# Optimization experiments

Hardware: AMD Instinct MI355X
Metric: run time of the kernel (lower is better)

Reference implementation:

```python
import jax, jax.numpy as jnp
import numpy as np

EPS = 1e-12  # torch f.normalize eps


def _rms_norm(x, g):
    # f.normalize(x, dim=1) * g * sqrt(C): L2-normalize over channel dim
    c = x.shape[1]
    n = jnp.maximum(jnp.linalg.norm(x, axis=1, keepdims=True), EPS)
    return x / n * g * (c ** 0.5)


def setup_inputs() -> dict:
    key = jax.random.key(0)
    ks = jax.random.split(key, 5)
    b, dim, H, W = 32, 256, 64, 64
    heads, dim_head, num_mem = 4, 32, 4
    hidden = heads * dim_head
    return {
        "x": jax.random.normal(ks[0], (b, dim, H, W), dtype=jnp.float32),
        "g1": jnp.ones((1, dim, 1, 1), dtype=jnp.float32),
        "mem_kv": jax.random.normal(ks[1], (2, heads, dim_head, num_mem), dtype=jnp.float32),
        "w_qkv": jax.random.normal(ks[2], (3 * hidden, dim), dtype=jnp.float32) * (1.0 / np.sqrt(dim)),
        "w_out": jax.random.normal(ks[3], (dim, hidden), dtype=jnp.float32) * (1.0 / np.sqrt(hidden)),
        "b_out": jnp.zeros((dim,), dtype=jnp.float32),
        "g2": jnp.ones((1, dim, 1, 1), dtype=jnp.float32),
    }


def reference(x, g1, mem_kv, w_qkv, w_out, b_out, g2):
    b, c, H, W = x.shape
    _, heads, dim_head, num_mem = mem_kv.shape
    n = H * W
    scale = dim_head ** -0.5

    xn = _rms_norm(x, g1)
    # 1x1 conv qkv projection: [b, 3*hidden, H, W]
    qkv = jnp.einsum('oc,bchw->bohw', w_qkv, xn)
    hidden = heads * dim_head
    q, k, v = jnp.split(qkv, 3, axis=1)
    # b (h d) x y -> b h d (x y)
    q = q.reshape(b, heads, dim_head, n)
    k = k.reshape(b, heads, dim_head, n)
    v = v.reshape(b, heads, dim_head, n)

    mk = jnp.broadcast_to(mem_kv[0], (b, heads, dim_head, num_mem))
    mv = jnp.broadcast_to(mem_kv[1], (b, heads, dim_head, num_mem))
    k = jnp.concatenate([mk, k], axis=-1)
    v = jnp.concatenate([mv, v], axis=-1)

    q = jax.nn.softmax(q, axis=-2) * scale  # softmax over head dim d
    k = jax.nn.softmax(k, axis=-1)          # softmax over sequence n

    context = jnp.einsum('bhdn,bhen->bhde', k, v)   # [b,h,d,e]
    out = jnp.einsum('bhde,bhdn->bhen', context, q)  # [b,h,e,n]
    out = out.reshape(b, hidden, H, W)

    o = jnp.einsum('oc,bchw->bohw', w_out, out) + b_out[None, :, None, None]
    return _rms_norm(o, g2)
```

## Files before the change

### kernel.cpp

```cpp
#include <hip/hip_runtime.h>
#include <math.h>

#define CC   256
#define HW   4096
#define OC3  384
#define HID  128
#define DH   32
#define NM   4
#define NPART 8
#define SCALE 0.17677669529663688f

typedef __bf16 bf16x8 __attribute__((ext_vector_type(8)));
typedef float  f32x4  __attribute__((ext_vector_type(4)));

__device__ __forceinline__ ushort f2bf(float x) {
    union { float f; unsigned u; } v; v.f = x;
    unsigned r = v.u + 0x7fffu + ((v.u >> 16) & 1u);
    return (ushort)(r >> 16);
}
__device__ __forceinline__ float bf2f(ushort b) {
    union { unsigned u; float f; } v; v.u = ((unsigned)b) << 16; return v.f;
}
__device__ __forceinline__ void g2l16(const void* g, void* l) {
    __builtin_amdgcn_global_load_lds(
        (const __attribute__((address_space(1))) void*)g,
        (__attribute__((address_space(3))) void*)l, 16, 0, 0);
}

__global__ __launch_bounds__(256) void k_xn(const float* __restrict__ x,
        const float* __restrict__ wqkv, const float* __restrict__ g1,
        const float* __restrict__ wout,
        ushort* __restrict__ wq2t, ushort* __restrict__ woutt,
        ushort* __restrict__ xnT) {
    __shared__ float xt[256 * 36];
    __shared__ float ps[8 * 33];
    __shared__ float invn[32];
    int tid = threadIdx.x;
    if (blockIdx.x < 384) {
        int o = blockIdx.x;
        wq2t[(size_t)o * CC + tid] = f2bf(wqkv[(size_t)o * CC + tid] * g1[tid] * 16.0f);
        if (o < CC && tid < HID) woutt[(size_t)o * HID + tid] = f2bf(wout[(size_t)o * HID + tid]);
    }
    int pix0 = blockIdx.x * 32;
    int b = pix0 >> 12, hw0 = pix0 & 4095;
    int p = tid & 31, cg = tid >> 5;
    const float* xb = x + (size_t)b * CC * HW + hw0;
    {
        int cr = tid >> 3;
        int chunk = tid & 7;
        #pragma unroll
        for (int pass = 0; pass < 8; ++pass) {
            int c = pass * 32 + cr;
            float4 v = *(const float4*)&xb[(size_t)c * HW + chunk * 4];
            *(float4*)&xt[c * 36 + chunk * 4] = v;
        }
    }
    __syncthreads();
    float s = 0.f;
    #pragma unroll 8
    for (int i = 0; i < 32; ++i) { float v = xt[(cg * 32 + i) * 36 + p]; s += v * v; }
    ps[cg * 33 + p] = s;
    __syncthreads();
    if (tid < 32) {
        float t = 0.f;
        #pragma unroll
        for (int g = 0; g < 8; ++g) t += ps[g * 33 + tid];
        invn[tid] = 1.0f / fmaxf(sqrtf(t), 1e-12f);
    }
    __syncthreads();
    float inv = invn[p];
    ushort* dst = xnT + ((size_t)(pix0 + p)) * CC + cg * 32;
    #pragma unroll
    for (int q = 0; q < 4; ++q) {
        uint4 pk; ushort* o8 = (ushort*)&pk;
        #pragma unroll
        for (int i = 0; i < 8; ++i) o8[i] = f2bf(xt[(cg * 32 + q * 8 + i) * 36 + p] * inv);
        *(uint4*)&dst[q * 8] = pk;
    }
}

__global__ __launch_bounds__(256) void k_qkv(const ushort* __restrict__ wq2t,
        const ushort* __restrict__ xnT, ushort* __restrict__ qkv) {
    __shared__ __align__(16) ushort As[2][128 * 32];
    __shared__ __align__(16) ushort Bs[2][128 * 32];
    int tid = threadIdx.x;
    int lin = blockIdx.x + 2 * (blockIdx.y + 32 * blockIdx.z);
    int swz = (lin & 7) * 256 + (lin >> 3);
    int m0 = 128 + (swz % 2) * 128;
    int t_ = swz / 2;
    int p0 = (t_ & 31) * 128;
    int b  = t_ >> 5;
    int lane = tid & 63, wid = tid >> 6;
    int l15 = tid & 15, quad = (tid >> 4) & 3;
    int wm = wid >> 1, wn = wid & 1;
    int rsub = lane >> 2;
    const ushort* Ab = wq2t + (size_t)m0 * CC;
    const ushort* Bb = xnT + ((size_t)(b * HW + p0)) * CC;
    f32x4 acc[4][4];
    #pragma unroll
    for (int i = 0; i < 4; ++i)
        #pragma unroll
        for (int j = 0; j < 4; ++j) acc[i][j] = (f32x4){0.f, 0.f, 0.f, 0.f};

    auto stage = [&](int buf, int k0) {
        #pragma unroll
        for (int q = 0; q < 2; ++q) {
            int rw = wid * 32 + q * 16;
            int r  = rw + rsub;
            int sc = (lane & 3) ^ ((r >> 1) & 3);
            g2l16(Ab + (size_t)r * CC + k0 + sc * 8, &As[buf][rw * 32]);
            g2l16(Bb + (size_t)r * CC + k0 + sc * 8, &Bs[buf][rw * 32]);
        }
    };

    stage(0, 0);
    __syncthreads();
    #pragma unroll
    for (int s = 0; s < 8; ++s) {
        int cur = s & 1;
        if (s < 7) stage(cur ^ 1, (s + 1) * 32);
        bf16x8 af[4], bfr[4];
        #pragma unroll
        for (int mt = 0; mt < 4; ++mt) {
            int ra = wm * 64 + mt * 16 + l15;
            af[mt] = *(const bf16x8*)&As[cur][ra * 32 + ((quad ^ ((ra >> 1) & 3)) << 3)];
        }
        #pragma unroll
        for (int nt = 0; nt < 4; ++nt) {
            int rb = wn * 64 + nt * 16 + l15;
            bfr[nt] = *(const bf16x8*)&Bs[cur][rb * 32 + ((quad ^ ((rb >> 1) & 3)) << 3)];
        }
        #pragma unroll
        for (int mt = 0; mt < 4; ++mt)
            #pragma unroll
            for (int nt = 0; nt < 4; ++nt)
                acc[mt][nt] = __builtin_amdgcn_mfma_f32_16x16x32_bf16(
                                  af[mt], bfr[nt], acc[mt][nt], 0, 0, 0);
        __syncthreads();
    }
    #pragma unroll
    for (int mt = 0; mt < 4; ++mt) {
        int o = m0 + wm * 64 + mt * 16 + quad * 4;
        #pragma unroll
        for (int nt = 0; nt < 4; ++nt) {
            int pix = p0 + wn * 64 + nt * 16 + l15;
            ushort* dst = qkv + ((size_t)(b * OC3 + o)) * HW + pix;
            #pragma unroll
            for (int r = 0; r < 4; ++r) dst[(size_t)r * HW] = f2bf(acc[mt][nt][r]);
        }
    }
}

__global__ void k_ksoft(const ushort* __restrict__ qkv, const float* __restrict__ memkv,
                        float* __restrict__ kmaxb, float* __restrict__ rsumb) {
    int row = blockIdx.x * 4 + (threadIdx.x >> 6);
    int lane = threadIdx.x & 63;
    int b = row >> 7, hd = row & 127;
    const ushort* kp = qkv + ((size_t)(b * OC3 + HID + hd)) * HW;
    uint4 kreg[8];
    #pragma unroll
    for (int i = 0; i < 8; ++i) kreg[i] = *(const uint4*)&kp[i * 512 + lane * 8];
    float m = -1e30f;
    #pragma unroll
    for (int i = 0; i < 8; ++i) {
        const ushort* e = (const ushort*)&kreg[i];
        #pragma unroll
        for (int j = 0; j < 8; ++j) m = fmaxf(m, bf2f(e[j]));
    }
    #pragma unroll
    for (int s = 1; s < 64; s <<= 1) m = fmaxf(m, __shfl_xor(m, s));
    const float* mk = memkv + hd * NM;
    #pragma unroll
    for (int j = 0; j < NM; ++j) m = fmaxf(m, mk[j]);
    float s = 0.f;
    #pragma unroll
    for (int i = 0; i < 8; ++i) {
        const ushort* e = (const ushort*)&kreg[i];
        #pragma unroll
        for (int j = 0; j < 8; ++j) s += __expf(bf2f(e[j]) - m);
    }
    #pragma unroll
    for (int t = 1; t < 64; t <<= 1) s += __shfl_xor(s, t);
    #pragma unroll
    for (int j = 0; j < NM; ++j) s += __expf(mk[j] - m);
    if (lane == 0) { kmaxb[row] = m; rsumb[row] = 1.0f / s; }
}

__global__ __launch_bounds__(256) void k_ctx(const ushort* __restrict__ qkv,
        const float* __restrict__ memkv, const float* __restrict__ kmaxb,
        const float* __restrict__ rsumb, float* __restrict__ ctxp) {
    __shared__ __align__(16) char smem[32768];
    ushort* klw = (ushort*)smem;
    ushort* vlw = (ushort*)(smem + 16384);
    float*  red = (float*)smem;
    int tid = threadIdx.x;
    int lane = tid & 63, wid = tid >> 6;
    int l15 = lane & 15, quad = lane >> 4;
    int bh = blockIdx.x, part = blockIdx.y;
    int b = bh >> 2, h = bh & 3;
    int rowbase = bh * DH;
    int r  = lane >> 1;
    int ch = (lane & 1) * 32;
    const ushort* kp = qkv + ((size_t)(b * OC3 + HID + h * DH) + r) * HW + part * 512;
    const ushort* vp = qkv + ((size_t)(b * OC3 + 2 * HID + h * DH) + r) * HW + part * 512;
    float kmr = kmaxb[rowbase + r], rsr = rsumb[rowbase + r];
    ushort* myk = klw + wid * 2048;
    ushort* myv = vlw + wid * 2048;
    f32x4 acc[2][2];
    #pragma unroll
    for (int i = 0; i < 2; ++i)
        #pragma unroll
        for (int j = 0; j < 2; ++j) acc[i][j] = (f32x4){0.f, 0.f, 0.f, 0.f};

    #pragma unroll
    for (int t = 0; t < 2; ++t) {
        int n0 = wid * 64 + t * 256;
        #pragma unroll
        for (int i = 0; i < 4; ++i) {
            uint4 kv4 = *(const uint4*)&kp[n0 + ch + i * 8];
            uint4 vv4 = *(const uint4*)&vp[n0 + ch + i * 8];
            uint4 ko; ushort* kw = (ushort*)&ko; const ushort* ke = (const ushort*)&kv4;
            #pragma unroll
            for (int j = 0; j < 8; ++j) kw[j] = f2bf(__expf(bf2f(ke[j]) - kmr) * rsr);
            int boff = ((ch + i * 8) * 2) ^ ((r & 7) << 4);
            *(uint4*)((char*)&myk[r * 64] + boff) = ko;
            *(uint4*)((char*)&myv[r * 64] + boff) = vv4;
        }
        #pragma unroll
        for (int ks = 0; ks < 2; ++ks) {
            bf16x8 af[2], bf[2];
            #pragma unroll
            for (int dt = 0; dt < 2; ++dt) {
                int row = dt * 16 + l15;
                int boff = (ks * 64 + quad * 16) ^ ((row & 7) << 4);
                af[dt] = *(const bf16x8*)((char*)&myk[row * 64] + boff);
                bf[dt] = *(const bf16x8*)((char*)&myv[row * 64] + boff);
            }
            #pragma unroll
            for (int dt = 0; dt < 2; ++dt)
                #pragma unroll
                for (int et = 0; et < 2; ++et)
                    acc[dt][et] = __builtin_amdgcn_mfma_f32_16x16x32_bf16(
                                      af[dt], bf[et], acc[dt][et], 0, 0, 0);
        }
    }
    __syncthreads();
    #pragma unroll
    for (int dt = 0; dt < 2; ++dt)
        #pragma unroll
        for (int et = 0; et < 2; ++et)
            #pragma unroll
            for (int rr = 0; rr < 4; ++rr) {
                int d = dt * 16 + quad * 4 + rr;
                int e = et * 16 + l15;
                red[wid * 1024 + d * 32 + e] = acc[dt][et][rr];
            }
    __syncthreads();
    {
        int o0 = tid * 4;
        f32x4 s4 = (f32x4){0.f, 0.f, 0.f, 0.f};
        #pragma unroll
        for (int w = 0; w < 4; ++w) {
            f32x4 v = *(const f32x4*)&red[w * 1024 + o0];
            s4[0] += v[0]; s4[1] += v[1]; s4[2] += v[2]; s4[3] += v[3];
        }
        if (part == 0) {
            int d = o0 >> 5;
            float km = kmaxb[rowbase + d], rsm = rsumb[rowbase + d];
            #pragma unroll
            for (int q = 0; q < 4; ++q) {
                int e = (o0 + q) & 31;
                #pragma unroll
                for (int m = 0; m < NM; ++m) {
                    float kw = __expf(memkv[(h * DH + d) * NM + m] - km) * rsm;
                    s4[q] += kw * memkv[512 + (h * DH + e) * NM + m];
                }
            }
        }
        *(f32x4*)&ctxp[(size_t)part * 131072 + (size_t)bh * 1024 + o0] = s4;
    }
}

__global__ __launch_bounds__(256) void k_w2(const float* __restrict__ ctxp,
        const ushort* __restrict__ woutt, ushort* __restrict__ W2) {
    __shared__ ushort ctxb[4 * 32 * 40];
    int tid = threadIdx.x, b = blockIdx.x;
    int wid = tid >> 6;
    int l15 = tid & 15, quad = (tid >> 4) & 3;
    #pragma unroll
    for (int j = 0; j < 16; ++j) {
        int idx = tid + j * 256;
        float s = 0.f;
        #pragma unroll
        for (int p = 0; p < NPART; ++p)
            s += ctxp[(size_t)p * 131072 + (size_t)b * 4096 + idx];
        int h = idx >> 10, d = (idx >> 5) & 31, e = idx & 31;
        ctxb[(h * 32 + d) * 40 + e] = f2bf(s);
    }
    __syncthreads();
    #pragma unroll
    for (int h = 0; h < 4; ++h) {
        f32x4 acc[4][2];
        #pragma unroll
        for (int i = 0; i < 4; ++i)
            #pragma unroll
            for (int j = 0; j < 2; ++j) acc[i][j] = (f32x4){0.f, 0.f, 0.f, 0.f};
        bf16x8 af[4], bfr[2];
        #pragma unroll
        for (int mt = 0; mt < 4; ++mt)
            af[mt] = *(const bf16x8*)&woutt[(size_t)(wid * 64 + mt * 16 + l15) * HID
                                            + h * DH + quad * 8];
        #pragma unroll
        for (int nt = 0; nt < 2; ++nt)
            bfr[nt] = *(const bf16x8*)&ctxb[(h * 32 + nt * 16 + l15) * 40 + quad * 8];
        #pragma unroll
        for (int mt = 0; mt < 4; ++mt)
            #pragma unroll
            for (int nt = 0; nt < 2; ++nt)
                acc[mt][nt] = __builtin_amdgcn_mfma_f32_16x16x32_bf16(
                                  af[mt], bfr[nt], acc[mt][nt], 0, 0, 0);
        #pragma unroll
        for (int mt = 0; mt < 4; ++mt)
            #pragma unroll
            for (int nt = 0; nt < 2; ++nt)
                #pragma unroll
                for (int r = 0; r < 4; ++r) {
                    int oc = wid * 64 + mt * 16 + quad * 4 + r;
                    int d  = nt * 16 + l15;
                    W2[((size_t)b * CC + oc) * HID + h * DH + d] = f2bf(acc[mt][nt][r]);
                }
    }
}

__global__ __launch_bounds__(256) void k_final(const ushort* __restrict__ xnT,
        const ushort* __restrict__ wq2t, const ushort* __restrict__ W2,
        const float* __restrict__ bout, const float* __restrict__ g2,
        float* __restrict__ y) {
    __shared__ __align__(16) char smem[52224];
    ushort* xnTs = (ushort*)smem;
    float*  red  = (float*)smem;
    float*  invs = (float*)(smem + 4352);
    ushort* Qw   = (ushort*)(smem + 16384);
    ushort* sq   = (ushort*)(smem + 32768);
    float*  bl   = (float*)(smem + 50176);
    float*  gl   = (float*)(smem + 51200);
    int tid = threadIdx.x;
    int b = blockIdx.y;
    int hwb = blockIdx.x * 64;
    int lane = tid & 63, wid = tid >> 6;
    int l15 = tid & 15, quad = (tid >> 4) & 3;
    int rsub = lane >> 2;
    bl[tid] = bout[tid];
    gl[tid] = g2[tid];

    auto stageX = [&](int half) {
        const ushort* xb = xnT + ((size_t)(b * HW + hwb)) * CC + half * 128;
        #pragma unroll
        for (int qq = 0; qq < 4; ++qq) {
            int r0 = qq * 16 + wid * 4;
            int r  = r0 + (lane >> 4);
            int g  = (lane & 15) ^ (r & 7);
            g2l16(xb + (size_t)r * CC + g * 8, &xnTs[r0 * 128]);
        }
    };
    auto stageQ = [&](int buf, int k0) {
        #pragma unroll
        for (int qq = 0; qq < 2; ++qq) {
            int rw = wid * 32 + qq * 16;
            int r  = rw + rsub;
            int sc = (lane & 3) ^ ((r >> 1) & 3);
            g2l16(wq2t + (size_t)r * CC + k0 + sc * 8, &Qw[buf * 4096 + rw * 32]);
        }
    };

    f32x4 accq[2][4];
    #pragma unroll
    for (int i = 0; i < 2; ++i)
        #pragma unroll
        for (int j = 0; j < 4; ++j) accq[i][j] = (f32x4){0.f, 0.f, 0.f, 0.f};
    stageX(0);
    stageQ(0, 0);
    __syncthreads();
    #pragma unroll
    for (int s = 0; s < 8; ++s) {
        int cur = s & 1;
        if (s < 7 && s != 3) stageQ(cur ^ 1, (s + 1) * 32);
        bf16x8 af[2], bfr[4];
        #pragma unroll
        for (int mt = 0; mt < 2; ++mt) {
            int ra = wid * 32 + mt * 16 + l15;
            af[mt] = *(const bf16x8*)&Qw[cur * 4096 + ra * 32 + ((quad ^ ((ra >> 1) & 3)) << 3)];
        }
        int cread = (s & 3) * 4 + quad;
        #pragma unroll
        for (int nt = 0; nt < 4; ++nt) {
            int rb = nt * 16 + l15;
            bfr[nt] = *(const bf16x8*)&xnTs[rb * 128 + ((cread ^ (rb & 7)) << 3)];
        }
        #pragma unroll
        for (int mt = 0; mt < 2; ++mt)
            #pragma unroll
            for (int nt = 0; nt < 4; ++nt)
                accq[mt][nt] = __builtin_amdgcn_mfma_f32_16x16x32_bf16(
                                   af[mt], bfr[nt], accq[mt][nt], 0, 0, 0);
        if (s == 3) {
            __syncthreads();
            stageX(1);
            stageQ(cur ^ 1, 128);
        }
        __syncthreads();
    }

    #pragma unroll
    for (int nt = 0; nt < 4; ++nt) {
        float m = -1e30f;
        #pragma unroll
        for (int mt = 0; mt < 2; ++mt)
            #pragma unroll
            for (int r = 0; r < 4; ++r) m = fmaxf(m, accq[mt][nt][r]);
        m = fmaxf(m, __shfl_xor(m, 16));
        m = fmaxf(m, __shfl_xor(m, 32));
        float s = 0.f;
        float e[2][4];
        #pragma unroll
        for (int mt = 0; mt < 2; ++mt)
            #pragma unroll
            for (int r = 0; r < 4; ++r) { e[mt][r] = __expf(accq[mt][nt][r] - m); s += e[mt][r]; }
        s += __shfl_xor(s, 16);
        s += __shfl_xor(s, 32);
        float r_ = SCALE / s;
        int pix = nt * 16 + l15;
        #pragma unroll
        for (int mt = 0; mt < 2; ++mt)
            #pragma unroll
            for (int r = 0; r < 4; ++r)
                sq[pix * 136 + wid * 32 + mt * 16 + quad * 4 + r] = f2bf(e[mt][r] * r_);
    }

    ushort* WsQ = Qw;
    f32x4 acc[4][4];
    #pragma unroll
    for (int i = 0; i < 4; ++i)
        #pragma unroll
        for (int j = 0; j < 4; ++j) acc[i][j] = (f32x4){0.f, 0.f, 0.f, 0.f};
    const ushort* W2b = W2 + (size_t)b * CC * HID;
    for (int k0 = 0; k0 < HID; k0 += 32) {
        __syncthreads();
        #pragma unroll
        for (int q = 0; q < 4; ++q) {
            int rw = wid * 64 + q * 16;
            int r  = rw + rsub;
            int sc = (lane & 3) ^ ((r >> 1) & 3);
            g2l16(W2b + (size_t)r * HID + k0 + sc * 8, &WsQ[rw * 32]);
        }
        __syncthreads();
        bf16x8 af[4], bfr[4];
        #pragma unroll
        for (int mt = 0; mt < 4; ++mt) {
            int ra = wid * 64 + mt * 16 + l15;
            af[mt] = *(const bf16x8*)&WsQ[ra * 32 + ((quad ^ ((ra >> 1) & 3)) << 3)];
        }
        #pragma unroll
        for (int nt = 0; nt < 4; ++nt)
            bfr[nt] = *(const bf16x8*)&sq[(nt * 16 + l15) * 136 + k0 + quad * 8];
        #pragma unroll
        for (int mt = 0; mt < 4; ++mt)
            #pragma unroll
            for (int nt = 0; nt < 4; ++nt)
                acc[mt][nt] = __builtin_amdgcn_mfma_f32_16x16x32_bf16(
                                  af[mt], bfr[nt], acc[mt][nt], 0, 0, 0);
    }

    float part[4] = {0.f, 0.f, 0.f, 0.f};
    #pragma unroll
    for (int mt = 0; mt < 4; ++mt)
        #pragma unroll
        for (int r = 0; r < 4; ++r) {
            int oc = wid * 64 + mt * 16 + quad * 4 + r;
            float bo = bl[oc];
            #pragma unroll
            for (int nt = 0; nt < 4; ++nt) {
                float v = acc[mt][nt][r] + bo;
                acc[mt][nt][r] = v;
                part[nt] += v * v;
            }
        }
    __syncthreads();
    #pragma unroll
    for (int nt = 0; nt < 4; ++nt)
        red[(nt * 16 + l15) * 17 + wid * 4 + quad] = part[nt];
    __syncthreads();
    if (tid < 64) {
        float s = 0.f;
        #pragma unroll
        for (int g = 0; g < 16; ++g) s += red[tid * 17 + g];
        invs[tid] = 1.0f / fmaxf(sqrtf(s), 1e-12f);
    }
    __syncthreads();
    #pragma unroll
    for (int mt = 0; mt < 4; ++mt)
        #pragma unroll
        for (int nt = 0; nt < 4; ++nt) {
            int pix = nt * 16 + l15;
            float iv = invs[pix];
            #pragma unroll
            for (int r = 0; r < 4; ++r) {
                int oc = wid * 64 + mt * 16 + quad * 4 + r;
                y[((size_t)(b * CC + oc)) * HW + hwb + pix] = acc[mt][nt][r] * iv * gl[oc] * 16.0f;
            }
        }
}

extern "C" void kernel_launch(void* const* d_in, const int* in_sizes, int n_in,
                              void* d_out, int out_size, void* d_ws, size_t ws_size,
                              hipStream_t stream) {
    const float* x     = (const float*)d_in[0];
    const float* g1    = (const float*)d_in[1];
    const float* memkv = (const float*)d_in[2];
    const float* wqkv  = (const float*)d_in[3];
    const float* wout  = (const float*)d_in[4];
    const float* bout  = (const float*)d_in[5];
    const float* g2    = (const float*)d_in[6];
    float* y = (float*)d_out;

    char* w = (char*)d_ws;
    ushort* wq2t  = (ushort*)w;  w += (size_t)OC3 * CC * 2;
    ushort* woutt = (ushort*)w;  w += (size_t)CC * HID * 2;
    float*  kmaxb = (float*)w;   w += 4096 * 4;
    float*  rsumb = (float*)w;   w += 4096 * 4;
    float*  ctxp  = (float*)w;   w += (size_t)NPART * 131072 * 4;
    ushort* W2    = (ushort*)w;  w += (size_t)32 * CC * HID * 2;
    ushort* xnT   = (ushort*)w;  w += (size_t)32 * HW * CC * 2;
    ushort* qkv   = (ushort*)w;  w += (size_t)32 * OC3 * HW * 2;

    k_xn    <<<dim3(4096),      dim3(256), 0, stream>>>(x, wqkv, g1, wout, wq2t, woutt, xnT);
    k_qkv   <<<dim3(2, 32, 32), dim3(256), 0, stream>>>(wq2t, xnT, qkv);
    k_ksoft <<<dim3(1024),      dim3(256), 0, stream>>>(qkv, memkv, kmaxb, rsumb);
    k_ctx   <<<dim3(128, 8),    dim3(256), 0, stream>>>(qkv, memkv, kmaxb, rsumb, ctxp);
    k_w2    <<<dim3(32),        dim3(256), 0, stream>>>(ctxp, woutt, W2);
    k_final <<<dim3(64, 32),    dim3(256), 0, stream>>>(xnT, wq2t, W2, bout, g2, y);
}
```

Measured before the change: 353.4 us.

## Fuse key softmax stats into context kernel with online per-partition rescaling

Removes the separate key-softmax statistics kernel. Each context block now computes its partition-local max and exp-sum for the keys and stores them. The context kernel accumulates exp(k - local max) times v without normalizing, and k_w2 merges the partitions with flash-style rescaling, folding in the memory key/value terms. This drops one launch and one full extra read of K, at the cost of an extra block barrier and a small reduction in k_w2.

```diff
diff --git a/kernel.cpp b/kernel.cpp
--- a/kernel.cpp
+++ b/kernel.cpp
@@ -151,77 +151,63 @@
     }
 }
 
-__global__ void k_ksoft(const ushort* __restrict__ qkv, const float* __restrict__ memkv,
-                        float* __restrict__ kmaxb, float* __restrict__ rsumb) {
-    int row = blockIdx.x * 4 + (threadIdx.x >> 6);
-    int lane = threadIdx.x & 63;
-    int b = row >> 7, hd = row & 127;
-    const ushort* kp = qkv + ((size_t)(b * OC3 + HID + hd)) * HW;
-    uint4 kreg[8];
-    #pragma unroll
-    for (int i = 0; i < 8; ++i) kreg[i] = *(const uint4*)&kp[i * 512 + lane * 8];
-    float m = -1e30f;
-    #pragma unroll
-    for (int i = 0; i < 8; ++i) {
-        const ushort* e = (const ushort*)&kreg[i];
-        #pragma unroll
-        for (int j = 0; j < 8; ++j) m = fmaxf(m, bf2f(e[j]));
-    }
-    #pragma unroll
-    for (int s = 1; s < 64; s <<= 1) m = fmaxf(m, __shfl_xor(m, s));
-    const float* mk = memkv + hd * NM;
-    #pragma unroll
-    for (int j = 0; j < NM; ++j) m = fmaxf(m, mk[j]);
-    float s = 0.f;
-    #pragma unroll
-    for (int i = 0; i < 8; ++i) {
-        const ushort* e = (const ushort*)&kreg[i];
-        #pragma unroll
-        for (int j = 0; j < 8; ++j) s += __expf(bf2f(e[j]) - m);
-    }
-    #pragma unroll
-    for (int t = 1; t < 64; t <<= 1) s += __shfl_xor(s, t);
-    #pragma unroll
-    for (int j = 0; j < NM; ++j) s += __expf(mk[j] - m);
-    if (lane == 0) { kmaxb[row] = m; rsumb[row] = 1.0f / s; }
-}
-
 __global__ __launch_bounds__(256) void k_ctx(const ushort* __restrict__ qkv,
-        const float* __restrict__ memkv, const float* __restrict__ kmaxb,
-        const float* __restrict__ rsumb, float* __restrict__ ctxp) {
+        float* __restrict__ ctxp, float* __restrict__ mstat, float* __restrict__ sstat) {
     __shared__ __align__(16) char smem[32768];
     ushort* klw = (ushort*)smem;
     ushort* vlw = (ushort*)(smem + 16384);
     float*  red = (float*)smem;
+    __shared__ float mred[4][32];
+    __shared__ float sred[4][32];
     int tid = threadIdx.x;
     int lane = tid & 63, wid = tid >> 6;
     int l15 = lane & 15, quad = lane >> 4;
     int bh = blockIdx.x, part = blockIdx.y;
     int b = bh >> 2, h = bh & 3;
-    int rowbase = bh * DH;
     int r  = lane >> 1;
     int ch = (lane & 1) * 32;
     const ushort* kp = qkv + ((size_t)(b * OC3 + HID + h * DH) + r) * HW + part * 512;
     const ushort* vp = qkv + ((size_t)(b * OC3 + 2 * HID + h * DH) + r) * HW + part * 512;
-    float kmr = kmaxb[rowbase + r], rsr = rsumb[rowbase + r];
     ushort* myk = klw + wid * 2048;
     ushort* myv = vlw + wid * 2048;
-    f32x4 acc[2][2];
-    #pragma unroll
-    for (int i = 0; i < 2; ++i)
-        #pragma unroll
-        for (int j = 0; j < 2; ++j) acc[i][j] = (f32x4){0.f, 0.f, 0.f, 0.f};
-
+
+    uint4 kreg[2][4];
+    float lm = -1e30f;
     #pragma unroll
     for (int t = 0; t < 2; ++t) {
         int n0 = wid * 64 + t * 256;
         #pragma unroll
         for (int i = 0; i < 4; ++i) {
-            uint4 kv4 = *(const uint4*)&kp[n0 + ch + i * 8];
+            kreg[t][i] = *(const uint4*)&kp[n0 + ch + i * 8];
+            const ushort* ke = (const ushort*)&kreg[t][i];
+            #pragma unroll
+            for (int j = 0; j < 8; ++j) lm = fmaxf(lm, bf2f(ke[j]));
+        }
+    }
+    lm = fmaxf(lm, __shfl_xor(lm, 1));
+    if ((lane & 1) == 0) mred[wid][r] = lm;
+    __syncthreads();
+    float mp = fmaxf(fmaxf(mred[0][r], mred[1][r]), fmaxf(mred[2][r], mred[3][r]));
+
+    f32x4 acc[2][2];
+    #pragma unroll
+    for (int i = 0; i < 2; ++i)
+        #pragma unroll
+        for (int j = 0; j < 2; ++j) acc[i][j] = (f32x4){0.f, 0.f, 0.f, 0.f};
+    float ls = 0.f;
+    #pragma unroll
+    for (int t = 0; t < 2; ++t) {
+        int n0 = wid * 64 + t * 256;
+        #pragma unroll
+        for (int i = 0; i < 4; ++i) {
             uint4 vv4 = *(const uint4*)&vp[n0 + ch + i * 8];
-            uint4 ko; ushort* kw = (ushort*)&ko; const ushort* ke = (const ushort*)&kv4;
-            #pragma unroll
-            for (int j = 0; j < 8; ++j) kw[j] = f2bf(__expf(bf2f(ke[j]) - kmr) * rsr);
+            uint4 ko; ushort* kw = (ushort*)&ko; const ushort* ke = (const ushort*)&kreg[t][i];
+            #pragma unroll
+            for (int j = 0; j < 8; ++j) {
+                float e = __expf(bf2f(ke[j]) - mp);
+                ls += e;
+                kw[j] = f2bf(e);
+            }
             int boff = ((ch + i * 8) * 2) ^ ((r & 7) << 4);
             *(uint4*)((char*)&myk[r * 64] + boff) = ko;
             *(uint4*)((char*)&myv[r * 64] + boff) = vv4;
@@ -244,7 +230,17 @@
                                       af[dt], bf[et], acc[dt][et], 0, 0, 0);
         }
     }
-    __syncthreads();
+    ls += __shfl_xor(ls, 1);
+    if ((lane & 1) == 0) sred[wid][r] = ls;
+    __syncthreads();
+    if (tid < 32) {
+        float s = sred[0][tid] + sred[1][tid] + sred[2][tid] + sred[3][tid];
+        float m2 = fmaxf(fmaxf(mred[0][tid], mred[1][tid]),
+                         fmaxf(mred[2][tid], mred[3][tid]));
+        size_t o = ((size_t)part * 128 + bh) * 32 + tid;
+        mstat[o] = m2;
+        sstat[o] = s;
+    }
     #pragma unroll
     for (int dt = 0; dt < 2; ++dt)
         #pragma unroll
@@ -264,37 +260,55 @@
             f32x4 v = *(const f32x4*)&red[w * 1024 + o0];
             s4[0] += v[0]; s4[1] += v[1]; s4[2] += v[2]; s4[3] += v[3];
         }
-        if (part == 0) {
-            int d = o0 >> 5;
-            float km = kmaxb[rowbase + d], rsm = rsumb[rowbase + d];
-            #pragma unroll
-            for (int q = 0; q < 4; ++q) {
-                int e = (o0 + q) & 31;
-                #pragma unroll
-                for (int m = 0; m < NM; ++m) {
-                    float kw = __expf(memkv[(h * DH + d) * NM + m] - km) * rsm;
-                    s4[q] += kw * memkv[512 + (h * DH + e) * NM + m];
-                }
-            }
-        }
         *(f32x4*)&ctxp[(size_t)part * 131072 + (size_t)bh * 1024 + o0] = s4;
     }
 }
 
 __global__ __launch_bounds__(256) void k_w2(const float* __restrict__ ctxp,
+        const float* __restrict__ mstat, const float* __restrict__ sstat,
+        const float* __restrict__ memkv,
         const ushort* __restrict__ woutt, ushort* __restrict__ W2) {
     __shared__ ushort ctxb[4 * 32 * 40];
+    __shared__ float scl[NPART][128];
+    __shared__ float memsc[128][NM];
     int tid = threadIdx.x, b = blockIdx.x;
     int wid = tid >> 6;
     int l15 = tid & 15, quad = (tid >> 4) & 3;
+    if (tid < 128) {
+        int h = tid >> 5, d = tid & 31;
+        size_t base = (size_t)(b * 4 + h) * 32 + d;
+        float mp[NPART];
+        float M = -1e30f;
+        #pragma unroll
+        for (int p = 0; p < NPART; ++p) { mp[p] = mstat[(size_t)p * 4096 + base]; M = fmaxf(M, mp[p]); }
+        float mk[NM];
+        #pragma unroll
+        for (int m = 0; m < NM; ++m) { mk[m] = memkv[(h * DH + d) * NM + m]; M = fmaxf(M, mk[m]); }
+        float Z = 0.f;
+        #pragma unroll
+        for (int p = 0; p < NPART; ++p) Z += sstat[(size_t)p * 4096 + base] * __expf(mp[p] - M);
+        #pragma unroll
+        for (int m = 0; m < NM; ++m) Z += __expf(mk[m] - M);
+        float iz = 1.0f / Z;
+        #pragma unroll
+        for (int p = 0; p < NPART; ++p) scl[p][tid] = __expf(mp[p] - M) * iz;
+        #pragma unroll
+        for (int m = 0; m < NM; ++m) memsc[tid][m] = __expf(mk[m] - M) * iz;
+    }
+    __syncthreads();
     #pragma unroll
     for (int j = 0; j < 16; ++j) {
         int idx = tid + j * 256;
+        int rr = idx >> 5;
+        int e  = idx & 31;
+        int h  = idx >> 10, d = (idx >> 5) & 31;
         float s = 0.f;
         #pragma unroll
         for (int p = 0; p < NPART; ++p)
-            s += ctxp[(size_t)p * 131072 + (size_t)b * 4096 + idx];
-        int h = idx >> 10, d = (idx >> 5) & 31, e = idx & 31;
+            s += ctxp[(size_t)p * 131072 + (size_t)b * 4096 + idx] * scl[p][rr];
+        #pragma unroll
+        for (int m = 0; m < NM; ++m)
+            s += memsc[rr][m] * memkv[512 + (h * DH + e) * NM + m];
         ctxb[(h * 32 + d) * 40 + e] = f2bf(s);
     }
     __syncthreads();
@@ -526,8 +540,8 @@
     char* w = (char*)d_ws;
     ushort* wq2t  = (ushort*)w;  w += (size_t)OC3 * CC * 2;
     ushort* woutt = (ushort*)w;  w += (size_t)CC * HID * 2;
-    float*  kmaxb = (float*)w;   w += 4096 * 4;
-    float*  rsumb = (float*)w;   w += 4096 * 4;
+    float*  mstat = (float*)w;   w += (size_t)NPART * 4096 * 4;
+    float*  sstat = (float*)w;   w += (size_t)NPART * 4096 * 4;
     float*  ctxp  = (float*)w;   w += (size_t)NPART * 131072 * 4;
     ushort* W2    = (ushort*)w;  w += (size_t)32 * CC * HID * 2;
     ushort* xnT   = (ushort*)w;  w += (size_t)32 * HW * CC * 2;
@@ -535,8 +549,7 @@
 
     k_xn    <<<dim3(4096),      dim3(256), 0, stream>>>(x, wqkv, g1, wout, wq2t, woutt, xnT);
     k_qkv   <<<dim3(2, 32, 32), dim3(256), 0, stream>>>(wq2t, xnT, qkv);
-    k_ksoft <<<dim3(1024),      dim3(256), 0, stream>>>(qkv, memkv, kmaxb, rsumb);
-    k_ctx   <<<dim3(128, 8),    dim3(256), 0, stream>>>(qkv, memkv, kmaxb, rsumb, ctxp);
-    k_w2    <<<dim3(32),        dim3(256), 0, stream>>>(ctxp, woutt, W2);
+    k_ctx   <<<dim3(128, 8),    dim3(256), 0, stream>>>(qkv, ctxp, mstat, sstat);
+    k_w2    <<<dim3(32),        dim3(256), 0, stream>>>(ctxp, mstat, sstat, memkv, woutt, W2);
     k_final <<<dim3(64, 32),    dim3(256), 0, stream>>>(xnT, wq2t, W2, bout, g2, y);
 }
```

Result: faster. 344.0 us (-2.7%).
